# Performance work log

Hardware: AMD Instinct MI355X
Metric: run time of the kernel (lower is better)

The kernel has to match this reference:

```python
import jax, jax.numpy as jnp
import numpy as np

B, S, D, H = 2, 2048, 1024, 16
DH = D // H
ROPE_BASE = 10000.0


def apply_rope(x):
    # x: [B, H, S, DH]; rotate-half RoPE, base 10000
    half = DH // 2
    inv_freq = 1.0 / (ROPE_BASE ** (jnp.arange(half, dtype=jnp.float32) / half))
    ang = jnp.arange(S, dtype=jnp.float32)[:, None] * inv_freq[None, :]  # [S, half]
    cos = jnp.cos(ang)[None, None]  # [1,1,S,half]
    sin = jnp.sin(ang)[None, None]
    x1, x2 = x[..., :half], x[..., half:]
    return jnp.concatenate([x1 * cos - x2 * sin, x1 * sin + x2 * cos], axis=-1)


def setup_inputs() -> dict:
    key = jax.random.key(0)
    ks = jax.random.split(key, 9)
    w = lambda k: jax.random.normal(k, (D, D), dtype=jnp.float32) * 0.02
    return {
        "x": jax.random.normal(ks[0], (B, S, D), dtype=jnp.float32),
        "Wq": w(ks[1]), "bq": jnp.zeros((D,), jnp.float32),
        "Wk": w(ks[2]), "bk": jnp.zeros((D,), jnp.float32),
        "Wv": w(ks[3]), "bv": jnp.zeros((D,), jnp.float32),
        "Wo": w(ks[4]), "bo": jnp.zeros((D,), jnp.float32),
    }


def reference(x, Wq, bq, Wk, bk, Wv, bv, Wo, bo):
    # projections (W stored as [in, out])
    q = x @ Wq + bq
    k = x @ Wk + bk
    v = x @ Wv + bv
    # [B, S, D] -> [B, H, S, DH]
    to_heads = lambda t: t.reshape(B, S, H, DH).transpose(0, 2, 1, 3)
    q, k, v = to_heads(q), to_heads(k), to_heads(v)
    q = apply_rope(q)
    k = apply_rope(k)
    scores = jnp.einsum("bhqd,bhkd->bhqk", q, k) / jnp.sqrt(jnp.float32(DH))
    causal = jnp.tril(jnp.ones((S, S), dtype=bool))  # [S, S]
    scores = jnp.where(causal[None, None], scores, -jnp.inf)
    probs = jax.nn.softmax(scores, axis=-1)
    ctx = jnp.einsum("bhqk,bhkd->bhqd", probs, v)
    ctx = ctx.transpose(0, 2, 1, 3).reshape(B, S, D)  # concat heads
    return ctx @ Wo + bo
```

## Files before the change

### kernel.cpp

```cpp
#include <hip/hip_runtime.h>
#include <hip/hip_bf16.h>

#define B_  2
#define S_  2048
#define D_  1024
#define H_  16
#define DH_ 64

typedef __attribute__((ext_vector_type(8))) short bf16x8;
typedef __attribute__((ext_vector_type(4))) float f32x4;

__device__ __forceinline__ short f2bf(float f) {
  unsigned int u; __builtin_memcpy(&u, &f, 4);
  u = (u + 0x7FFFu + ((u >> 16) & 1u)) >> 16;
  return (short)u;
}
__device__ __forceinline__ unsigned cvtpk(float a, float b) {
  unsigned r;
  asm("v_cvt_pk_bf16_f32 %0, %1, %2" : "=v"(r) : "v"(a), "v"(b));
  return r;
}

#define GLOAD_LDS16(gp, lp) \
  __builtin_amdgcn_global_load_lds((const __attribute__((address_space(1))) void*)(gp), \
                                   (__attribute__((address_space(3))) void*)(lp), 16, 0, 0)

#define MFMA16(a, b, c) __builtin_amdgcn_mfma_f32_16x16x32_bf16(a, b, c, 0, 0, 0)

union U8 { unsigned u[4]; bf16x8 v; };

__global__ __launch_bounds__(256) void k_cvt(const float* __restrict__ in,
                                             short* __restrict__ out, int n4) {
  int i = blockIdx.x * 256 + threadIdx.x;
  if (i >= n4) return;
  float4 v = ((const float4*)in)[i];
  short4 o; o.x = f2bf(v.x); o.y = f2bf(v.y); o.z = f2bf(v.z); o.w = f2bf(v.w);
  *(short4*)(out + (size_t)i * 4) = o;
}

__global__ __launch_bounds__(256) void k_transpose4(const float* __restrict__ W0,
                                                    const float* __restrict__ W1,
                                                    const float* __restrict__ W2,
                                                    const float* __restrict__ W3,
                                                    short* __restrict__ WtBase) {
  __shared__ float tile[32][33];
  const float* W = (blockIdx.z == 0) ? W0 : (blockIdx.z == 1) ? W1 :
                   (blockIdx.z == 2) ? W2 : W3;
  short* Wt = WtBase + (size_t)blockIdx.z * D_ * D_;
  int tx = threadIdx.x, ty = threadIdx.y;
  int bx = blockIdx.x * 32, by = blockIdx.y * 32;
  #pragma unroll
  for (int i = 0; i < 32; i += 8)
    tile[ty + i][tx] = W[(size_t)(by + ty + i) * D_ + bx + tx];
  __syncthreads();
  #pragma unroll
  for (int i = 0; i < 32; i += 8)
    Wt[(size_t)(bx + ty + i) * D_ + by + tx] = f2bf(tile[tx][ty + i]);
}

__global__ __launch_bounds__(256) void k_rope_table(float* __restrict__ cosT,
                                                    float* __restrict__ sinT) {
  int i = blockIdx.x * 256 + threadIdx.x;
  int s = i >> 5, d = i & 31;
  float invf = exp2f(-(float)d * (13.287712379549449f / 32.0f));
  float ang = (float)s * invf;
  cosT[i] = cosf(ang);
  sinT[i] = sinf(ang);
}

__global__ __launch_bounds__(256) void k_gemm_qkv(const short* __restrict__ A,
                                                  const short* __restrict__ Bt,
                                                  const float* __restrict__ bq,
                                                  const float* __restrict__ bk,
                                                  const float* __restrict__ bv,
                                                  const float* __restrict__ cosT,
                                                  const float* __restrict__ sinT,
                                                  short* __restrict__ qb,
                                                  short* __restrict__ kb,
                                                  short* __restrict__ vb) {
  const int K = 1024;
  __shared__ __align__(16) short lA[128 * 32];
  __shared__ __align__(16) short lB[128 * 32];
  const int tid = threadIdx.x;
  const int wid = tid >> 6, lane = tid & 63;
  const int brow = blockIdx.y * 128, bcol = blockIdx.x * 128;
  const int wr = wid >> 1, wc = wid & 1;
  const int g = lane >> 4, c15 = lane & 15;
  const int sr = lane >> 2, scol = (lane & 3) * 8;
  f32x4 acc[4][4] = {};

  for (int kt = 0; kt < K; kt += 32) {
    __syncthreads();
    #pragma unroll
    for (int ch = 0; ch < 2; ++ch) {
      const short* ga = A + (size_t)(brow + ch * 64 + wid * 16 + sr) * K + kt + scol;
      const short* gb = Bt + (size_t)(bcol + ch * 64 + wid * 16 + sr) * K + kt + scol;
      GLOAD_LDS16(ga, &lA[(ch * 64 + wid * 16) * 32]);
      GLOAD_LDS16(gb, &lB[(ch * 64 + wid * 16) * 32]);
    }
    __syncthreads();
    bf16x8 af[4], bfr[4];
    #pragma unroll
    for (int mi = 0; mi < 4; ++mi)
      af[mi] = *(const bf16x8*)&lA[(wr * 64 + mi * 16 + c15) * 32 + g * 8];
    #pragma unroll
    for (int ni = 0; ni < 4; ++ni)
      bfr[ni] = *(const bf16x8*)&lB[(wc * 64 + ni * 16 + c15) * 32 + g * 8];
    #pragma unroll
    for (int mi = 0; mi < 4; ++mi)
      #pragma unroll
      for (int ni = 0; ni < 4; ++ni)
        acc[mi][ni] = MFMA16(af[mi], bfr[ni], acc[mi][ni]);
  }

  const int seg = bcol >> 10;
  const float* bp = (seg == 0) ? bq : (seg == 1) ? bk : bv;
  short* dst = (seg == 0) ? qb : (seg == 1) ? kb : vb;
  const float alpha = (seg == 0) ? 0.18033688f : 1.0f;
  const bool rope = (seg < 2);
  #pragma unroll
  for (int mi = 0; mi < 4; ++mi) {
    #pragma unroll
    for (int ni = 0; ni < 2; ++ni) {
      int col  = bcol + wc * 64 + ni * 16 + c15;
      int lcol = col & 1023;
      int d    = col & 63;
      float b1 = bp[lcol], b2 = bp[lcol + 32];
      #pragma unroll
      for (int r = 0; r < 4; ++r) {
        int row = brow + wr * 64 + mi * 16 + g * 4 + r;
        float x1 = (acc[mi][ni][r]     + b1) * alpha;
        float x2 = (acc[mi][ni + 2][r] + b2) * alpha;
        float o1 = x1, o2 = x2;
        if (rope) {
          int s = row & (S_ - 1);
          float co = cosT[s * 32 + d], si = sinT[s * 32 + d];
          o1 = x1 * co - x2 * si;
          o2 = x1 * si + x2 * co;
        }
        dst[(size_t)row * 1024 + lcol]      = f2bf(o1);
        dst[(size_t)row * 1024 + lcol + 32] = f2bf(o2);
      }
    }
  }
}

__global__ __launch_bounds__(256) void k_gemm(const short* __restrict__ A,
                                              const short* __restrict__ Bt,
                                              const float* __restrict__ bias,
                                              float* __restrict__ out,
                                              int M, int N, int K) {
  __shared__ __align__(16) short lA[128 * 32];
  __shared__ __align__(16) short lB[128 * 32];
  const int tid = threadIdx.x;
  const int wid = tid >> 6, lane = tid & 63;
  const int brow = blockIdx.y * 128, bcol = blockIdx.x * 128;
  const int wr = wid >> 1, wc = wid & 1;
  const int g = lane >> 4, c15 = lane & 15;
  const int sr = lane >> 2, scol = (lane & 3) * 8;
  f32x4 acc[4][4] = {};

  for (int kt = 0; kt < K; kt += 32) {
    __syncthreads();
    #pragma unroll
    for (int ch = 0; ch < 2; ++ch) {
      const short* ga = A + (size_t)(brow + ch * 64 + wid * 16 + sr) * K + kt + scol;
      const short* gb = Bt + (size_t)(bcol + ch * 64 + wid * 16 + sr) * K + kt + scol;
      GLOAD_LDS16(ga, &lA[(ch * 64 + wid * 16) * 32]);
      GLOAD_LDS16(gb, &lB[(ch * 64 + wid * 16) * 32]);
    }
    __syncthreads();
    bf16x8 af[4], bfr[4];
    #pragma unroll
    for (int mi = 0; mi < 4; ++mi)
      af[mi] = *(const bf16x8*)&lA[(wr * 64 + mi * 16 + c15) * 32 + g * 8];
    #pragma unroll
    for (int ni = 0; ni < 4; ++ni)
      bfr[ni] = *(const bf16x8*)&lB[(wc * 64 + ni * 16 + c15) * 32 + g * 8];
    #pragma unroll
    for (int mi = 0; mi < 4; ++mi)
      #pragma unroll
      for (int ni = 0; ni < 4; ++ni)
        acc[mi][ni] = MFMA16(af[mi], bfr[ni], acc[mi][ni]);
  }

  #pragma unroll
  for (int mi = 0; mi < 4; ++mi) {
    #pragma unroll
    for (int ni = 0; ni < 4; ++ni) {
      int col = bcol + wc * 64 + ni * 16 + c15;
      float bv = bias[col];
      #pragma unroll
      for (int r = 0; r < 4; ++r) {
        int row = brow + wr * 64 + mi * 16 + g * 4 + r;
        out[(size_t)row * N + col] = acc[mi][ni][r] + bv;
      }
    }
  }
}

__global__ __launch_bounds__(256) void k_flash(const short* __restrict__ Qb,
                                               const short* __restrict__ Kb,
                                               const short* __restrict__ Vb,
                                               short* __restrict__ Ctx,
                                               float* __restrict__ pO,
                                               float* __restrict__ pML) {
  __shared__ __align__(16) short Vt[2][64][72];
  __shared__ __align__(16) short Kl[2][4096];
  const int bid = blockIdx.x;
  const int sched = bid >> 5, bh = bid & 31;
  int qt, t0, t1, sid = 0; bool split;
  if (sched < 19) { qt = 18 - sched; t0 = 0; t1 = qt; split = false; }
  else {
    int j = sched - 19; qt = 31 - (j >> 1);
    int h1 = (qt + 2) >> 1;
    if ((j & 1) == 0) { t0 = h1; t1 = qt; }
    else              { t0 = 0;  t1 = h1 - 1; }
    split = true; sid = bh * 26 + j;
  }
  const int b   = bh >> 4, h = bh & 15;
  const int tid = threadIdx.x, w = tid >> 6, lane = tid & 63;
  const int g   = lane >> 4, c15 = lane & 15;
  const int qg0 = qt * 64 + w * 16;
  const int qabs = qg0 + c15;

  const short* qp = Qb + ((size_t)(b * S_ + qabs)) * D_ + h * DH_ + g * 8;
  bf16x8 qf0 = *(const bf16x8*)qp;
  bf16x8 qf1 = *(const bf16x8*)(qp + 32);

  const int vkv = lane;
  const int vd0 = w * 16;
  const int vcol = vkv ^ (w << 3);
  const short* vrow = Vb + (size_t)b * S_ * D_ + h * DH_ + vd0;

  const short* kbase = Kb + (size_t)b * S_ * D_ + h * DH_;
  const int kidx0 = w * 128 + lane;
  const int kkv0 = kidx0 >> 3, kdb0 = (kidx0 & 7) ^ (kkv0 & 7);
  const int kidx1 = kidx0 + 64;
  const int kkv1 = kidx1 >> 3, kdb1 = (kidx1 & 7) ^ (kkv1 & 7);

  f32x4 o[4] = {};
  float m = -1e30f, l = 0.0f;

  {
    const short* kb0 = kbase + (size_t)(t0 * 64) * D_;
    GLOAD_LDS16(kb0 + (size_t)kkv0 * D_ + kdb0 * 8, &Kl[t0 & 1][(w * 128) * 8]);
    GLOAD_LDS16(kb0 + (size_t)kkv1 * D_ + kdb1 * 8, &Kl[t0 & 1][(w * 128 + 64) * 8]);
    const short* vp = vrow + (size_t)(t0 * 64 + vkv) * D_;
    bf16x8 a = *(const bf16x8*)vp;
    bf16x8 c = *(const bf16x8*)(vp + 8);
    #pragma unroll
    for (int j = 0; j < 8; ++j) Vt[t0 & 1][vd0 + j][vcol] = a[j];
    #pragma unroll
    for (int j = 0; j < 8; ++j) Vt[t0 & 1][vd0 + 8 + j][vcol] = c[j];
  }
  __syncthreads();

  for (int t = t0; t <= t1; ++t) {
    const int kv0 = t * 64;
    bf16x8 nv0, nv1;
    if (t + 1 <= t1) {
      const short* kb2 = kbase + (size_t)(kv0 + 64) * D_;
      GLOAD_LDS16(kb2 + (size_t)kkv0 * D_ + kdb0 * 8, &Kl[(t + 1) & 1][(w * 128) * 8]);
      GLOAD_LDS16(kb2 + (size_t)kkv1 * D_ + kdb1 * 8, &Kl[(t + 1) & 1][(w * 128 + 64) * 8]);
      const short* vp = vrow + (size_t)(kv0 + 64 + vkv) * D_;
      nv0 = *(const bf16x8*)vp;
      nv1 = *(const bf16x8*)(vp + 8);
    }
    const short* ks = &Kl[t & 1][0];
    f32x4 s[4] = {};
    __builtin_amdgcn_s_setprio(1);
    #pragma unroll
    for (int n = 0; n < 4; ++n) {
      int krow = (n * 16 + c15) * 64;
      bf16x8 k0 = *(const bf16x8*)&ks[krow + ((g ^ (c15 & 7)) * 8)];
      bf16x8 k1 = *(const bf16x8*)&ks[krow + (((g + 4) ^ (c15 & 7)) * 8)];
      s[n] = MFMA16(k0, qf0, s[n]);
      s[n] = MFMA16(k1, qf1, s[n]);
    }
    __builtin_amdgcn_s_setprio(0);
    if (kv0 + 63 > qg0) {
      #pragma unroll
      for (int n = 0; n < 4; ++n)
        #pragma unroll
        for (int r = 0; r < 4; ++r)
          if (kv0 + n * 16 + g * 4 + r > qabs) s[n][r] = -1e30f;
    }
    float pm = -1e30f;
    #pragma unroll
    for (int n = 0; n < 4; ++n)
      #pragma unroll
      for (int r = 0; r < 4; ++r) pm = fmaxf(pm, s[n][r]);
    pm = fmaxf(pm, __shfl_xor(pm, 16));
    pm = fmaxf(pm, __shfl_xor(pm, 32));
    if (!__all(pm <= m + 8.0f)) {
      float nm = fmaxf(m, pm);
      float corr = exp2f(m - nm);
      m = nm; l *= corr;
      float cf[4];
      #pragma unroll
      for (int r = 0; r < 4; ++r) cf[r] = __shfl(corr, g * 4 + r);
      #pragma unroll
      for (int dblk = 0; dblk < 4; ++dblk)
        #pragma unroll
        for (int r = 0; r < 4; ++r) o[dblk][r] *= cf[r];
    }
    float rs = 0.0f;
    #pragma unroll
    for (int n = 0; n < 4; ++n)
      #pragma unroll
      for (int r = 0; r < 4; ++r) {
        float p = exp2f(s[n][r] - m);
        s[n][r] = p; rs += p;
      }
    rs += __shfl_xor(rs, 16);
    rs += __shfl_xor(rs, 32);
    l += rs;
    unsigned pk[4][2];
    #pragma unroll
    for (int n = 0; n < 4; ++n) {
      pk[n][0] = cvtpk(s[n][0], s[n][1]);
      pk[n][1] = cvtpk(s[n][2], s[n][3]);
    }
    U8 pa[2];
    #pragma unroll
    for (int kh = 0; kh < 2; ++kh) {
      #pragma unroll
      for (int widx = 0; widx < 4; ++widx) {
        int src = (2 * (g & 1) + (widx >> 1)) * 16 + c15;
        unsigned lo = __shfl(pk[2 * kh][widx & 1], src);
        unsigned hi = __shfl(pk[2 * kh + 1][widx & 1], src);
        pa[kh].u[widx] = (g & 2) ? hi : lo;
      }
    }
    __builtin_amdgcn_s_setprio(1);
    #pragma unroll
    for (int kh = 0; kh < 2; ++kh)
      #pragma unroll
      for (int dblk = 0; dblk < 4; ++dblk) {
        bf16x8 vbf = *(const bf16x8*)&Vt[t & 1][dblk * 16 + c15][kh * 32 + ((g ^ dblk) * 8)];
        o[dblk] = MFMA16(pa[kh].v, vbf, o[dblk]);
      }
    __builtin_amdgcn_s_setprio(0);
    if (t + 1 <= t1) {
      #pragma unroll
      for (int j = 0; j < 8; ++j) Vt[(t + 1) & 1][vd0 + j][vcol] = nv0[j];
      #pragma unroll
      for (int j = 0; j < 8; ++j) Vt[(t + 1) & 1][vd0 + 8 + j][vcol] = nv1[j];
    }
    __syncthreads();
  }

  if (!split) {
    float linv = 1.0f / l;
    float lf[4];
    #pragma unroll
    for (int r = 0; r < 4; ++r) lf[r] = __shfl(linv, g * 4 + r);
    #pragma unroll
    for (int dblk = 0; dblk < 4; ++dblk)
      #pragma unroll
      for (int r = 0; r < 4; ++r) {
        int q = qg0 + g * 4 + r;
        Ctx[((size_t)(b * S_ + q)) * D_ + h * DH_ + dblk * 16 + c15] = f2bf(o[dblk][r] * lf[r]);
      }
  } else {
    float* po = pO + ((size_t)sid * 64 + w * 16) * 64;
    #pragma unroll
    for (int dblk = 0; dblk < 4; ++dblk)
      #pragma unroll
      for (int r = 0; r < 4; ++r)
        po[(g * 4 + r) * 64 + dblk * 16 + c15] = o[dblk][r];
    if (lane < 16) {
      pML[(size_t)sid * 128 + w * 16 + lane]      = m;
      pML[(size_t)sid * 128 + 64 + w * 16 + lane] = l;
    }
  }
}

__global__ __launch_bounds__(256) void k_combine(const float* __restrict__ pO,
                                                 const float* __restrict__ pML,
                                                 short* __restrict__ Ctx) {
  const int p = blockIdx.x;
  const int qt = 19 + (p >> 5), bh = p & 31;
  const int b = bh >> 4, h = bh & 15;
  const int jb = (31 - qt) * 2;
  const int sidB = bh * 26 + jb;
  const int sidA = bh * 26 + jb + 1;
  const int q = threadIdx.x >> 2;
  const int d0 = (threadIdx.x & 3) * 16;
  float mA = pML[(size_t)sidA * 128 + q], lA = pML[(size_t)sidA * 128 + 64 + q];
  float mB = pML[(size_t)sidB * 128 + q], lB = pML[(size_t)sidB * 128 + 64 + q];
  float M = fmaxf(mA, mB);
  float wA = exp2f(mA - M), wB = exp2f(mB - M);
  float inv = 1.0f / (lA * wA + lB * wB);
  const float* oA = pO + ((size_t)sidA * 64 + q) * 64 + d0;
  const float* oB = pO + ((size_t)sidB * 64 + q) * 64 + d0;
  short* cp = Ctx + ((size_t)(b * S_ + qt * 64 + q)) * D_ + h * DH_ + d0;
  #pragma unroll
  for (int i = 0; i < 16; i += 4) {
    float4 a = *(const float4*)(oA + i);
    float4 c = *(const float4*)(oB + i);
    cp[i + 0] = f2bf((a.x * wA + c.x * wB) * inv);
    cp[i + 1] = f2bf((a.y * wA + c.y * wB) * inv);
    cp[i + 2] = f2bf((a.z * wA + c.z * wB) * inv);
    cp[i + 3] = f2bf((a.w * wA + c.w * wB) * inv);
  }
}

extern "C" void kernel_launch(void* const* d_in, const int* in_sizes, int n_in,
                              void* d_out, int out_size, void* d_ws, size_t ws_size,
                              hipStream_t stream) {
  (void)in_sizes; (void)n_in; (void)out_size; (void)ws_size;
  const float* x  = (const float*)d_in[0];
  const float* Wq = (const float*)d_in[1];
  const float* bq = (const float*)d_in[2];
  const float* Wk = (const float*)d_in[3];
  const float* bk = (const float*)d_in[4];
  const float* Wv = (const float*)d_in[5];
  const float* bv = (const float*)d_in[6];
  const float* Wo = (const float*)d_in[7];
  const float* bo = (const float*)d_in[8];
  float* out = (float*)d_out;
  char* ws = (char*)d_ws;

  const size_t MS = (size_t)B_ * S_;
  short* xb  = (short*)(ws);
  short* wqT = (short*)(ws + (size_t)8 * 1024 * 1024);
  short* wkT = wqT + (size_t)D_ * D_;
  short* wvT = wkT + (size_t)D_ * D_;
  short* woT = wvT + (size_t)D_ * D_;
  short* qb  = (short*)(ws + (size_t)16 * 1024 * 1024);
  short* kb  = qb + MS * D_;
  short* vb  = kb + MS * D_;
  short* ctx = vb + MS * D_;
  float* cosT = (float*)(ws + (size_t)48 * 1024 * 1024);
  float* sinT = cosT + (size_t)S_ * 32;
  float* pO  = (float*)(ws);
  float* pML = (float*)(ws + (size_t)48 * 1024 * 1024 + 512 * 1024);

  k_cvt<<<dim3((unsigned)(MS * D_ / 4 / 256)), 256, 0, stream>>>(x, xb, (int)(MS * D_ / 4));
  k_transpose4<<<dim3(32, 32, 4), dim3(32, 8), 0, stream>>>(Wq, Wk, Wv, Wo, wqT);
  k_rope_table<<<dim3(S_ * 32 / 256), 256, 0, stream>>>(cosT, sinT);
  k_gemm_qkv<<<dim3(24, 32), 256, 0, stream>>>(xb, wqT, bq, bk, bv, cosT, sinT, qb, kb, vb);
  k_flash<<<dim3(45 * 32), 256, 0, stream>>>(qb, kb, vb, ctx, pO, pML);
  k_combine<<<dim3(13 * 32), 256, 0, stream>>>(pO, pML, ctx);
  k_gemm<<<dim3(8, 32), 256, 0, stream>>>(ctx, woT, bo, out, 4096, 1024, 1024);
}
```

Before: 138.5 us.

## Deepen flash K/V prefetch, swizzle GEMM tiles, merge prep kernels

```diff
diff --git a/kernel.cpp b/kernel.cpp
--- a/kernel.cpp
+++ b/kernel.cpp
@@ -27,15 +27,32 @@
 
 #define MFMA16(a, b, c) __builtin_amdgcn_mfma_f32_16x16x32_bf16(a, b, c, 0, 0, 0)
 
+#define RAW_BARRIER() do {                                   \
+    asm volatile("s_waitcnt lgkmcnt(0)" ::: "memory");       \
+    __builtin_amdgcn_s_barrier();                            \
+    asm volatile("" ::: "memory");                           \
+  } while (0)
+
 union U8 { unsigned u[4]; bf16x8 v; };
 
-__global__ __launch_bounds__(256) void k_cvt(const float* __restrict__ in,
-                                             short* __restrict__ out, int n4) {
-  int i = blockIdx.x * 256 + threadIdx.x;
-  if (i >= n4) return;
-  float4 v = ((const float4*)in)[i];
-  short4 o; o.x = f2bf(v.x); o.y = f2bf(v.y); o.z = f2bf(v.z); o.w = f2bf(v.w);
-  *(short4*)(out + (size_t)i * 4) = o;
+__global__ __launch_bounds__(256) void k_cvt_table(const float* __restrict__ in,
+                                                   short* __restrict__ out,
+                                                   float* __restrict__ cosT,
+                                                   float* __restrict__ sinT) {
+  int bid = blockIdx.x;
+  if (bid < 4096) {
+    int i = bid * 256 + threadIdx.x;
+    float4 v = ((const float4*)in)[i];
+    short4 o; o.x = f2bf(v.x); o.y = f2bf(v.y); o.z = f2bf(v.z); o.w = f2bf(v.w);
+    *(short4*)(out + (size_t)i * 4) = o;
+  } else {
+    int i = (bid - 4096) * 256 + threadIdx.x;
+    int s = i >> 5, d = i & 31;
+    float invf = exp2f(-(float)d * (13.287712379549449f / 32.0f));
+    float ang = (float)s * invf;
+    cosT[i] = cosf(ang);
+    sinT[i] = sinf(ang);
+  }
 }
 
 __global__ __launch_bounds__(256) void k_transpose4(const float* __restrict__ W0,
@@ -56,16 +73,6 @@
   #pragma unroll
   for (int i = 0; i < 32; i += 8)
     Wt[(size_t)(bx + ty + i) * D_ + by + tx] = f2bf(tile[tx][ty + i]);
-}
-
-__global__ __launch_bounds__(256) void k_rope_table(float* __restrict__ cosT,
-                                                    float* __restrict__ sinT) {
-  int i = blockIdx.x * 256 + threadIdx.x;
-  int s = i >> 5, d = i & 31;
-  float invf = exp2f(-(float)d * (13.287712379549449f / 32.0f));
-  float ang = (float)s * invf;
-  cosT[i] = cosf(ang);
-  sinT[i] = sinf(ang);
 }
 
 __global__ __launch_bounds__(256) void k_gemm_qkv(const short* __restrict__ A,
@@ -81,9 +88,12 @@
   const int K = 1024;
   __shared__ __align__(16) short lA[128 * 32];
   __shared__ __align__(16) short lB[128 * 32];
+  const int fid = blockIdx.y * 24 + blockIdx.x;
+  const int swz = (fid & 7) * 96 + (fid >> 3);
+  const int bxs = swz % 24, bys = swz / 24;
   const int tid = threadIdx.x;
   const int wid = tid >> 6, lane = tid & 63;
-  const int brow = blockIdx.y * 128, bcol = blockIdx.x * 128;
+  const int brow = bys * 128, bcol = bxs * 128;
   const int wr = wid >> 1, wc = wid & 1;
   const int g = lane >> 4, c15 = lane & 15;
   const int sr = lane >> 2, scol = (lane & 3) * 8;
@@ -152,9 +162,12 @@
                                               int M, int N, int K) {
   __shared__ __align__(16) short lA[128 * 32];
   __shared__ __align__(16) short lB[128 * 32];
+  const int fid = blockIdx.y * 8 + blockIdx.x;
+  const int swz = (fid & 7) * 32 + (fid >> 3);
+  const int bxs = swz % 8, bys = swz / 8;
   const int tid = threadIdx.x;
   const int wid = tid >> 6, lane = tid & 63;
-  const int brow = blockIdx.y * 128, bcol = blockIdx.x * 128;
+  const int brow = bys * 128, bcol = bxs * 128;
   const int wr = wid >> 1, wc = wid & 1;
   const int g = lane >> 4, c15 = lane & 15;
   const int sr = lane >> 2, scol = (lane & 3) * 8;
@@ -199,12 +212,66 @@
   }
 }
 
-__global__ __launch_bounds__(256) void k_flash(const short* __restrict__ Qb,
-                                               const short* __restrict__ Kb,
-                                               const short* __restrict__ Vb,
-                                               short* __restrict__ Ctx,
-                                               float* __restrict__ pO,
-                                               float* __restrict__ pML) {
+__device__ __forceinline__ void softmax_g(f32x4 (&s)[4], float& m, float& l,
+                                          f32x4 (&o)[4], int g) {
+  float pm = -1e30f;
+  #pragma unroll
+  for (int n = 0; n < 4; ++n)
+    #pragma unroll
+    for (int r = 0; r < 4; ++r) pm = fmaxf(pm, s[n][r]);
+  pm = fmaxf(pm, __shfl_xor(pm, 16));
+  pm = fmaxf(pm, __shfl_xor(pm, 32));
+  if (!__all(pm <= m + 8.0f)) {
+    float nm = fmaxf(m, pm);
+    float corr = exp2f(m - nm);
+    m = nm; l *= corr;
+    float cf[4];
+    #pragma unroll
+    for (int r = 0; r < 4; ++r) cf[r] = __shfl(corr, g * 4 + r);
+    #pragma unroll
+    for (int dblk = 0; dblk < 4; ++dblk)
+      #pragma unroll
+      for (int r = 0; r < 4; ++r) o[dblk][r] *= cf[r];
+  }
+  float rs = 0.0f;
+  #pragma unroll
+  for (int n = 0; n < 4; ++n)
+    #pragma unroll
+    for (int r = 0; r < 4; ++r) {
+      float p = exp2f(s[n][r] - m);
+      s[n][r] = p; rs += p;
+    }
+  rs += __shfl_xor(rs, 16);
+  rs += __shfl_xor(rs, 32);
+  l += rs;
+}
+
+__device__ __forceinline__ void build_pa(const f32x4 (&s)[4], U8 (&pa)[2],
+                                         int g, int c15) {
+  unsigned pk[4][2];
+  #pragma unroll
+  for (int n = 0; n < 4; ++n) {
+    pk[n][0] = cvtpk(s[n][0], s[n][1]);
+    pk[n][1] = cvtpk(s[n][2], s[n][3]);
+  }
+  #pragma unroll
+  for (int kh = 0; kh < 2; ++kh) {
+    #pragma unroll
+    for (int widx = 0; widx < 4; ++widx) {
+      int src = (2 * (g & 1) + (widx >> 1)) * 16 + c15;
+      unsigned lo = __shfl(pk[2 * kh][widx & 1], src);
+      unsigned hi = __shfl(pk[2 * kh + 1][widx & 1], src);
+      pa[kh].u[widx] = (g & 2) ? hi : lo;
+    }
+  }
+}
+
+__global__ __launch_bounds__(256, 4) void k_flash(const short* __restrict__ Qb,
+                                                  const short* __restrict__ Kb,
+                                                  const short* __restrict__ Vb,
+                                                  short* __restrict__ Ctx,
+                                                  float* __restrict__ pO,
+                                                  float* __restrict__ pML) {
   __shared__ __align__(16) short Vt[2][64][72];
   __shared__ __align__(16) short Kl[2][4096];
   const int bid = blockIdx.x;
@@ -242,114 +309,95 @@
   f32x4 o[4] = {};
   float m = -1e30f, l = 0.0f;
 
+  bf16x8 kc0, kc1, vc0, vc1, kn0, kn1, vn0, vn1;
+
   {
     const short* kb0 = kbase + (size_t)(t0 * 64) * D_;
-    GLOAD_LDS16(kb0 + (size_t)kkv0 * D_ + kdb0 * 8, &Kl[t0 & 1][(w * 128) * 8]);
-    GLOAD_LDS16(kb0 + (size_t)kkv1 * D_ + kdb1 * 8, &Kl[t0 & 1][(w * 128 + 64) * 8]);
+    bf16x8 tk0 = *(const bf16x8*)(kb0 + (size_t)kkv0 * D_ + kdb0 * 8);
+    bf16x8 tk1 = *(const bf16x8*)(kb0 + (size_t)kkv1 * D_ + kdb1 * 8);
     const short* vp = vrow + (size_t)(t0 * 64 + vkv) * D_;
-    bf16x8 a = *(const bf16x8*)vp;
-    bf16x8 c = *(const bf16x8*)(vp + 8);
-    #pragma unroll
-    for (int j = 0; j < 8; ++j) Vt[t0 & 1][vd0 + j][vcol] = a[j];
-    #pragma unroll
-    for (int j = 0; j < 8; ++j) Vt[t0 & 1][vd0 + 8 + j][vcol] = c[j];
-  }
-  __syncthreads();
-
-  for (int t = t0; t <= t1; ++t) {
-    const int kv0 = t * 64;
-    bf16x8 nv0, nv1;
-    if (t + 1 <= t1) {
-      const short* kb2 = kbase + (size_t)(kv0 + 64) * D_;
-      GLOAD_LDS16(kb2 + (size_t)kkv0 * D_ + kdb0 * 8, &Kl[(t + 1) & 1][(w * 128) * 8]);
-      GLOAD_LDS16(kb2 + (size_t)kkv1 * D_ + kdb1 * 8, &Kl[(t + 1) & 1][(w * 128 + 64) * 8]);
-      const short* vp = vrow + (size_t)(kv0 + 64 + vkv) * D_;
-      nv0 = *(const bf16x8*)vp;
-      nv1 = *(const bf16x8*)(vp + 8);
-    }
-    const short* ks = &Kl[t & 1][0];
-    f32x4 s[4] = {};
-    __builtin_amdgcn_s_setprio(1);
-    #pragma unroll
-    for (int n = 0; n < 4; ++n) {
-      int krow = (n * 16 + c15) * 64;
-      bf16x8 k0 = *(const bf16x8*)&ks[krow + ((g ^ (c15 & 7)) * 8)];
-      bf16x8 k1 = *(const bf16x8*)&ks[krow + (((g + 4) ^ (c15 & 7)) * 8)];
-      s[n] = MFMA16(k0, qf0, s[n]);
-      s[n] = MFMA16(k1, qf1, s[n]);
-    }
-    __builtin_amdgcn_s_setprio(0);
-    if (kv0 + 63 > qg0) {
-      #pragma unroll
-      for (int n = 0; n < 4; ++n)
-        #pragma unroll
-        for (int r = 0; r < 4; ++r)
-          if (kv0 + n * 16 + g * 4 + r > qabs) s[n][r] = -1e30f;
-    }
-    float pm = -1e30f;
-    #pragma unroll
-    for (int n = 0; n < 4; ++n)
-      #pragma unroll
-      for (int r = 0; r < 4; ++r) pm = fmaxf(pm, s[n][r]);
-    pm = fmaxf(pm, __shfl_xor(pm, 16));
-    pm = fmaxf(pm, __shfl_xor(pm, 32));
-    if (!__all(pm <= m + 8.0f)) {
-      float nm = fmaxf(m, pm);
-      float corr = exp2f(m - nm);
-      m = nm; l *= corr;
-      float cf[4];
-      #pragma unroll
-      for (int r = 0; r < 4; ++r) cf[r] = __shfl(corr, g * 4 + r);
-      #pragma unroll
-      for (int dblk = 0; dblk < 4; ++dblk)
-        #pragma unroll
-        for (int r = 0; r < 4; ++r) o[dblk][r] *= cf[r];
-    }
-    float rs = 0.0f;
-    #pragma unroll
-    for (int n = 0; n < 4; ++n)
-      #pragma unroll
-      for (int r = 0; r < 4; ++r) {
-        float p = exp2f(s[n][r] - m);
-        s[n][r] = p; rs += p;
-      }
-    rs += __shfl_xor(rs, 16);
-    rs += __shfl_xor(rs, 32);
-    l += rs;
-    unsigned pk[4][2];
-    #pragma unroll
-    for (int n = 0; n < 4; ++n) {
-      pk[n][0] = cvtpk(s[n][0], s[n][1]);
-      pk[n][1] = cvtpk(s[n][2], s[n][3]);
-    }
-    U8 pa[2];
-    #pragma unroll
-    for (int kh = 0; kh < 2; ++kh) {
-      #pragma unroll
-      for (int widx = 0; widx < 4; ++widx) {
-        int src = (2 * (g & 1) + (widx >> 1)) * 16 + c15;
-        unsigned lo = __shfl(pk[2 * kh][widx & 1], src);
-        unsigned hi = __shfl(pk[2 * kh + 1][widx & 1], src);
-        pa[kh].u[widx] = (g & 2) ? hi : lo;
-      }
-    }
-    __builtin_amdgcn_s_setprio(1);
-    #pragma unroll
-    for (int kh = 0; kh < 2; ++kh)
-      #pragma unroll
-      for (int dblk = 0; dblk < 4; ++dblk) {
-        bf16x8 vbf = *(const bf16x8*)&Vt[t & 1][dblk * 16 + c15][kh * 32 + ((g ^ dblk) * 8)];
-        o[dblk] = MFMA16(pa[kh].v, vbf, o[dblk]);
-      }
-    __builtin_amdgcn_s_setprio(0);
-    if (t + 1 <= t1) {
-      #pragma unroll
-      for (int j = 0; j < 8; ++j) Vt[(t + 1) & 1][vd0 + j][vcol] = nv0[j];
-      #pragma unroll
-      for (int j = 0; j < 8; ++j) Vt[(t + 1) & 1][vd0 + 8 + j][vcol] = nv1[j];
-    }
-    __syncthreads();
-  }
+    bf16x8 tv0 = *(const bf16x8*)vp;
+    bf16x8 tv1 = *(const bf16x8*)(vp + 8);
+    *(bf16x8*)&Kl[t0 & 1][kidx0 * 8] = tk0;
+    *(bf16x8*)&Kl[t0 & 1][kidx1 * 8] = tk1;
+    #pragma unroll
+    for (int j = 0; j < 8; ++j) Vt[t0 & 1][vd0 + j][vcol] = tv0[j];
+    #pragma unroll
+    for (int j = 0; j < 8; ++j) Vt[t0 & 1][vd0 + 8 + j][vcol] = tv1[j];
+    if (t0 + 1 <= t1) {
+      const short* kb1 = kbase + (size_t)((t0 + 1) * 64) * D_;
+      kc0 = *(const bf16x8*)(kb1 + (size_t)kkv0 * D_ + kdb0 * 8);
+      kc1 = *(const bf16x8*)(kb1 + (size_t)kkv1 * D_ + kdb1 * 8);
+      const short* vp1 = vrow + (size_t)((t0 + 1) * 64 + vkv) * D_;
+      vc0 = *(const bf16x8*)vp1;
+      vc1 = *(const bf16x8*)(vp1 + 8);
+    }
+  }
+  RAW_BARRIER();
+
+#define FBODY(T, KC0, KC1, VC0, VC1, KN0, KN1, VN0, VN1) do {                   \
+    const int kv0 = (T) * 64;                                                   \
+    if ((T) + 2 <= t1) {                                                        \
+      const short* kb2 = kbase + (size_t)(kv0 + 128) * D_;                      \
+      KN0 = *(const bf16x8*)(kb2 + (size_t)kkv0 * D_ + kdb0 * 8);               \
+      KN1 = *(const bf16x8*)(kb2 + (size_t)kkv1 * D_ + kdb1 * 8);               \
+      const short* vp2 = vrow + (size_t)(kv0 + 128 + vkv) * D_;                 \
+      VN0 = *(const bf16x8*)vp2;                                                \
+      VN1 = *(const bf16x8*)(vp2 + 8);                                          \
+    }                                                                           \
+    if (kv0 <= qg0 + 15) {                                                      \
+      const short* ks = &Kl[(T) & 1][0];                                        \
+      f32x4 s[4] = {};                                                          \
+      __builtin_amdgcn_s_setprio(1);                                            \
+      _Pragma("unroll")                                                         \
+      for (int n = 0; n < 4; ++n) {                                             \
+        int krow = (n * 16 + c15) * 64;                                         \
+        bf16x8 k0 = *(const bf16x8*)&ks[krow + ((g ^ (c15 & 7)) * 8)];          \
+        bf16x8 k1 = *(const bf16x8*)&ks[krow + (((g + 4) ^ (c15 & 7)) * 8)];    \
+        s[n] = MFMA16(k0, qf0, s[n]);                                           \
+        s[n] = MFMA16(k1, qf1, s[n]);                                           \
+      }                                                                         \
+      __builtin_amdgcn_s_setprio(0);                                            \
+      if (kv0 + 63 > qg0) {                                                     \
+        _Pragma("unroll")                                                       \
+        for (int n = 0; n < 4; ++n)                                             \
+          _Pragma("unroll")                                                     \
+          for (int r = 0; r < 4; ++r)                                           \
+            if (kv0 + n * 16 + g * 4 + r > qabs) s[n][r] = -1e30f;              \
+      }                                                                         \
+      softmax_g(s, m, l, o, g);                                                 \
+      U8 pa[2];                                                                 \
+      build_pa(s, pa, g, c15);                                                  \
+      __builtin_amdgcn_s_setprio(1);                                            \
+      _Pragma("unroll")                                                         \
+      for (int kh = 0; kh < 2; ++kh)                                            \
+        _Pragma("unroll")                                                       \
+        for (int dblk = 0; dblk < 4; ++dblk) {                                  \
+          bf16x8 vbf = *(const bf16x8*)&Vt[(T) & 1][dblk * 16 + c15]            \
+                                         [kh * 32 + ((g ^ dblk) * 8)];          \
+          o[dblk] = MFMA16(pa[kh].v, vbf, o[dblk]);                             \
+        }                                                                       \
+      __builtin_amdgcn_s_setprio(0);                                            \
+    }                                                                           \
+    if ((T) + 1 <= t1) {                                                        \
+      *(bf16x8*)&Kl[((T) + 1) & 1][kidx0 * 8] = KC0;                            \
+      *(bf16x8*)&Kl[((T) + 1) & 1][kidx1 * 8] = KC1;                            \
+      _Pragma("unroll")                                                         \
+      for (int j = 0; j < 8; ++j) Vt[((T) + 1) & 1][vd0 + j][vcol] = VC0[j];    \
+      _Pragma("unroll")                                                         \
+      for (int j = 0; j < 8; ++j) Vt[((T) + 1) & 1][vd0 + 8 + j][vcol] = VC1[j];\
+      RAW_BARRIER();                                                            \
+    }                                                                           \
+  } while (0)
+
+  for (int t = t0; t <= t1; ) {
+    FBODY(t, kc0, kc1, vc0, vc1, kn0, kn1, vn0, vn1);
+    ++t;
+    if (t > t1) break;
+    FBODY(t, kn0, kn1, vn0, vn1, kc0, kc1, vc0, vc1);
+    ++t;
+  }
+#undef FBODY
 
   if (!split) {
     float linv = 1.0f / l;
@@ -438,9 +486,8 @@
   float* pO  = (float*)(ws);
   float* pML = (float*)(ws + (size_t)48 * 1024 * 1024 + 512 * 1024);
 
-  k_cvt<<<dim3((unsigned)(MS * D_ / 4 / 256)), 256, 0, stream>>>(x, xb, (int)(MS * D_ / 4));
+  k_cvt_table<<<dim3(4096 + 256), 256, 0, stream>>>(x, xb, cosT, sinT);
   k_transpose4<<<dim3(32, 32, 4), dim3(32, 8), 0, stream>>>(Wq, Wk, Wv, Wo, wqT);
-  k_rope_table<<<dim3(S_ * 32 / 256), 256, 0, stream>>>(cosT, sinT);
   k_gemm_qkv<<<dim3(24, 32), 256, 0, stream>>>(xb, wqT, bq, bk, bv, cosT, sinT, qb, kb, vb);
   k_flash<<<dim3(45 * 32), 256, 0, stream>>>(qb, kb, vb, ctx, pO, pML);
   k_combine<<<dim3(13 * 32), 256, 0, stream>>>(pO, pML, ctx);
```

Result: faster. 135.6 us, median of 2 (-2.1%).

## Merge cvt and rope kernels, swizzle GEMM grids, single-buffer flash attention

Applied to the files above, without the earlier changes.

```diff
diff --git a/kernel.cpp b/kernel.cpp
--- a/kernel.cpp
+++ b/kernel.cpp
@@ -27,15 +27,37 @@
 
 #define MFMA16(a, b, c) __builtin_amdgcn_mfma_f32_16x16x32_bf16(a, b, c, 0, 0, 0)
 
+#define RAW_BARRIER() do {                                   \
+    asm volatile("s_waitcnt lgkmcnt(0)" ::: "memory");       \
+    __builtin_amdgcn_s_barrier();                            \
+    asm volatile("" ::: "memory");                           \
+  } while (0)
+#define PLAIN_BARRIER() do {                                 \
+    asm volatile("" ::: "memory");                           \
+    __builtin_amdgcn_s_barrier();                            \
+    asm volatile("" ::: "memory");                           \
+  } while (0)
+
 union U8 { unsigned u[4]; bf16x8 v; };
 
-__global__ __launch_bounds__(256) void k_cvt(const float* __restrict__ in,
-                                             short* __restrict__ out, int n4) {
-  int i = blockIdx.x * 256 + threadIdx.x;
-  if (i >= n4) return;
-  float4 v = ((const float4*)in)[i];
-  short4 o; o.x = f2bf(v.x); o.y = f2bf(v.y); o.z = f2bf(v.z); o.w = f2bf(v.w);
-  *(short4*)(out + (size_t)i * 4) = o;
+__global__ __launch_bounds__(256) void k_cvt_table(const float* __restrict__ in,
+                                                   short* __restrict__ out,
+                                                   float* __restrict__ cosT,
+                                                   float* __restrict__ sinT) {
+  int bid = blockIdx.x;
+  if (bid < 4096) {
+    int i = bid * 256 + threadIdx.x;
+    float4 v = ((const float4*)in)[i];
+    short4 o; o.x = f2bf(v.x); o.y = f2bf(v.y); o.z = f2bf(v.z); o.w = f2bf(v.w);
+    *(short4*)(out + (size_t)i * 4) = o;
+  } else {
+    int i = (bid - 4096) * 256 + threadIdx.x;
+    int s = i >> 5, d = i & 31;
+    float invf = exp2f(-(float)d * (13.287712379549449f / 32.0f));
+    float ang = (float)s * invf;
+    cosT[i] = cosf(ang);
+    sinT[i] = sinf(ang);
+  }
 }
 
 __global__ __launch_bounds__(256) void k_transpose4(const float* __restrict__ W0,
@@ -56,16 +78,6 @@
   #pragma unroll
   for (int i = 0; i < 32; i += 8)
     Wt[(size_t)(bx + ty + i) * D_ + by + tx] = f2bf(tile[tx][ty + i]);
-}
-
-__global__ __launch_bounds__(256) void k_rope_table(float* __restrict__ cosT,
-                                                    float* __restrict__ sinT) {
-  int i = blockIdx.x * 256 + threadIdx.x;
-  int s = i >> 5, d = i & 31;
-  float invf = exp2f(-(float)d * (13.287712379549449f / 32.0f));
-  float ang = (float)s * invf;
-  cosT[i] = cosf(ang);
-  sinT[i] = sinf(ang);
 }
 
 __global__ __launch_bounds__(256) void k_gemm_qkv(const short* __restrict__ A,
@@ -81,9 +93,12 @@
   const int K = 1024;
   __shared__ __align__(16) short lA[128 * 32];
   __shared__ __align__(16) short lB[128 * 32];
+  const int fid = blockIdx.y * 24 + blockIdx.x;
+  const int swz = (fid & 7) * 96 + (fid >> 3);
+  const int bxs = swz % 24, bys = swz / 24;
   const int tid = threadIdx.x;
   const int wid = tid >> 6, lane = tid & 63;
-  const int brow = blockIdx.y * 128, bcol = blockIdx.x * 128;
+  const int brow = bys * 128, bcol = bxs * 128;
   const int wr = wid >> 1, wc = wid & 1;
   const int g = lane >> 4, c15 = lane & 15;
   const int sr = lane >> 2, scol = (lane & 3) * 8;
@@ -152,9 +167,12 @@
                                               int M, int N, int K) {
   __shared__ __align__(16) short lA[128 * 32];
   __shared__ __align__(16) short lB[128 * 32];
+  const int fid = blockIdx.y * 8 + blockIdx.x;
+  const int swz = (fid & 7) * 32 + (fid >> 3);
+  const int bxs = swz % 8, bys = swz / 8;
   const int tid = threadIdx.x;
   const int wid = tid >> 6, lane = tid & 63;
-  const int brow = blockIdx.y * 128, bcol = blockIdx.x * 128;
+  const int brow = bys * 128, bcol = bxs * 128;
   const int wr = wid >> 1, wc = wid & 1;
   const int g = lane >> 4, c15 = lane & 15;
   const int sr = lane >> 2, scol = (lane & 3) * 8;
@@ -199,14 +217,68 @@
   }
 }
 
-__global__ __launch_bounds__(256) void k_flash(const short* __restrict__ Qb,
-                                               const short* __restrict__ Kb,
-                                               const short* __restrict__ Vb,
-                                               short* __restrict__ Ctx,
-                                               float* __restrict__ pO,
-                                               float* __restrict__ pML) {
-  __shared__ __align__(16) short Vt[2][64][72];
-  __shared__ __align__(16) short Kl[2][4096];
+__device__ __forceinline__ void softmax_g(f32x4 (&s)[4], float& m, float& l,
+                                          f32x4 (&o)[4], int g) {
+  float pm = -1e30f;
+  #pragma unroll
+  for (int n = 0; n < 4; ++n)
+    #pragma unroll
+    for (int r = 0; r < 4; ++r) pm = fmaxf(pm, s[n][r]);
+  pm = fmaxf(pm, __shfl_xor(pm, 16));
+  pm = fmaxf(pm, __shfl_xor(pm, 32));
+  if (!__all(pm <= m + 8.0f)) {
+    float nm = fmaxf(m, pm);
+    float corr = exp2f(m - nm);
+    m = nm; l *= corr;
+    float cf[4];
+    #pragma unroll
+    for (int r = 0; r < 4; ++r) cf[r] = __shfl(corr, g * 4 + r);
+    #pragma unroll
+    for (int dblk = 0; dblk < 4; ++dblk)
+      #pragma unroll
+      for (int r = 0; r < 4; ++r) o[dblk][r] *= cf[r];
+  }
+  float rs = 0.0f;
+  #pragma unroll
+  for (int n = 0; n < 4; ++n)
+    #pragma unroll
+    for (int r = 0; r < 4; ++r) {
+      float p = exp2f(s[n][r] - m);
+      s[n][r] = p; rs += p;
+    }
+  rs += __shfl_xor(rs, 16);
+  rs += __shfl_xor(rs, 32);
+  l += rs;
+}
+
+__device__ __forceinline__ void build_pa(const f32x4 (&s)[4], U8 (&pa)[2],
+                                         int g, int c15) {
+  unsigned pk[4][2];
+  #pragma unroll
+  for (int n = 0; n < 4; ++n) {
+    pk[n][0] = cvtpk(s[n][0], s[n][1]);
+    pk[n][1] = cvtpk(s[n][2], s[n][3]);
+  }
+  #pragma unroll
+  for (int kh = 0; kh < 2; ++kh) {
+    #pragma unroll
+    for (int widx = 0; widx < 4; ++widx) {
+      int src = (2 * (g & 1) + (widx >> 1)) * 16 + c15;
+      unsigned lo = __shfl(pk[2 * kh][widx & 1], src);
+      unsigned hi = __shfl(pk[2 * kh + 1][widx & 1], src);
+      pa[kh].u[widx] = (g & 2) ? hi : lo;
+    }
+  }
+}
+
+__global__ __launch_bounds__(256, 8) void k_flash(const short* __restrict__ Qb,
+                                                  const short* __restrict__ Kb,
+                                                  const short* __restrict__ Vb,
+                                                  short* __restrict__ Ctx,
+                                                  float* __restrict__ pO,
+                                                  float* __restrict__ pML) {
+  __shared__ __align__(16) short Vt[64][64];
+  __shared__ __align__(16) short Kl[4096];
   const int bid = blockIdx.x;
   const int sched = bid >> 5, bh = bid & 31;
   int qt, t0, t1, sid = 0; bool split;
@@ -228,9 +300,7 @@
   bf16x8 qf0 = *(const bf16x8*)qp;
   bf16x8 qf1 = *(const bf16x8*)(qp + 32);
 
-  const int vkv = lane;
   const int vd0 = w * 16;
-  const int vcol = vkv ^ (w << 3);
   const short* vrow = Vb + (size_t)b * S_ * D_ + h * DH_ + vd0;
 
   const short* kbase = Kb + (size_t)b * S_ * D_ + h * DH_;
@@ -242,113 +312,77 @@
   f32x4 o[4] = {};
   float m = -1e30f, l = 0.0f;
 
+  bf16x8 kc0, kc1, vc0, vc1;
+
   {
     const short* kb0 = kbase + (size_t)(t0 * 64) * D_;
-    GLOAD_LDS16(kb0 + (size_t)kkv0 * D_ + kdb0 * 8, &Kl[t0 & 1][(w * 128) * 8]);
-    GLOAD_LDS16(kb0 + (size_t)kkv1 * D_ + kdb1 * 8, &Kl[t0 & 1][(w * 128 + 64) * 8]);
-    const short* vp = vrow + (size_t)(t0 * 64 + vkv) * D_;
-    bf16x8 a = *(const bf16x8*)vp;
-    bf16x8 c = *(const bf16x8*)(vp + 8);
-    #pragma unroll
-    for (int j = 0; j < 8; ++j) Vt[t0 & 1][vd0 + j][vcol] = a[j];
-    #pragma unroll
-    for (int j = 0; j < 8; ++j) Vt[t0 & 1][vd0 + 8 + j][vcol] = c[j];
-  }
-  __syncthreads();
+    bf16x8 tk0 = *(const bf16x8*)(kb0 + (size_t)kkv0 * D_ + kdb0 * 8);
+    bf16x8 tk1 = *(const bf16x8*)(kb0 + (size_t)kkv1 * D_ + kdb1 * 8);
+    const short* vp = vrow + (size_t)(t0 * 64 + lane) * D_;
+    bf16x8 tv0 = *(const bf16x8*)vp;
+    bf16x8 tv1 = *(const bf16x8*)(vp + 8);
+    *(bf16x8*)&Kl[kidx0 * 8] = tk0;
+    *(bf16x8*)&Kl[kidx1 * 8] = tk1;
+    #pragma unroll
+    for (int j = 0; j < 8; ++j) Vt[vd0 + j][lane ^ ((j & 7) << 3)] = tv0[j];
+    #pragma unroll
+    for (int j = 0; j < 8; ++j) Vt[vd0 + 8 + j][lane ^ ((j & 7) << 3)] = tv1[j];
+  }
+  RAW_BARRIER();
 
   for (int t = t0; t <= t1; ++t) {
     const int kv0 = t * 64;
-    bf16x8 nv0, nv1;
     if (t + 1 <= t1) {
-      const short* kb2 = kbase + (size_t)(kv0 + 64) * D_;
-      GLOAD_LDS16(kb2 + (size_t)kkv0 * D_ + kdb0 * 8, &Kl[(t + 1) & 1][(w * 128) * 8]);
-      GLOAD_LDS16(kb2 + (size_t)kkv1 * D_ + kdb1 * 8, &Kl[(t + 1) & 1][(w * 128 + 64) * 8]);
-      const short* vp = vrow + (size_t)(kv0 + 64 + vkv) * D_;
-      nv0 = *(const bf16x8*)vp;
-      nv1 = *(const bf16x8*)(vp + 8);
-    }
-    const short* ks = &Kl[t & 1][0];
-    f32x4 s[4] = {};
-    __builtin_amdgcn_s_setprio(1);
-    #pragma unroll
-    for (int n = 0; n < 4; ++n) {
-      int krow = (n * 16 + c15) * 64;
-      bf16x8 k0 = *(const bf16x8*)&ks[krow + ((g ^ (c15 & 7)) * 8)];
-      bf16x8 k1 = *(const bf16x8*)&ks[krow + (((g + 4) ^ (c15 & 7)) * 8)];
-      s[n] = MFMA16(k0, qf0, s[n]);
-      s[n] = MFMA16(k1, qf1, s[n]);
-    }
-    __builtin_amdgcn_s_setprio(0);
-    if (kv0 + 63 > qg0) {
-      #pragma unroll
-      for (int n = 0; n < 4; ++n)
+      const short* kb1 = kbase + (size_t)(kv0 + 64) * D_;
+      kc0 = *(const bf16x8*)(kb1 + (size_t)kkv0 * D_ + kdb0 * 8);
+      kc1 = *(const bf16x8*)(kb1 + (size_t)kkv1 * D_ + kdb1 * 8);
+      const short* vp1 = vrow + (size_t)(kv0 + 64 + lane) * D_;
+      vc0 = *(const bf16x8*)vp1;
+      vc1 = *(const bf16x8*)(vp1 + 8);
+    }
+    if (kv0 <= qg0 + 15) {
+      f32x4 s[4] = {};
+      __builtin_amdgcn_s_setprio(1);
+      #pragma unroll
+      for (int n = 0; n < 4; ++n) {
+        int krow = (n * 16 + c15) * 64;
+        bf16x8 k0 = *(const bf16x8*)&Kl[krow + ((g ^ (c15 & 7)) * 8)];
+        bf16x8 k1 = *(const bf16x8*)&Kl[krow + (((g + 4) ^ (c15 & 7)) * 8)];
+        s[n] = MFMA16(k0, qf0, s[n]);
+        s[n] = MFMA16(k1, qf1, s[n]);
+      }
+      __builtin_amdgcn_s_setprio(0);
+      if (kv0 + 63 > qg0) {
         #pragma unroll
-        for (int r = 0; r < 4; ++r)
-          if (kv0 + n * 16 + g * 4 + r > qabs) s[n][r] = -1e30f;
-    }
-    float pm = -1e30f;
-    #pragma unroll
-    for (int n = 0; n < 4; ++n)
-      #pragma unroll
-      for (int r = 0; r < 4; ++r) pm = fmaxf(pm, s[n][r]);
-    pm = fmaxf(pm, __shfl_xor(pm, 16));
-    pm = fmaxf(pm, __shfl_xor(pm, 32));
-    if (!__all(pm <= m + 8.0f)) {
-      float nm = fmaxf(m, pm);
-      float corr = exp2f(m - nm);
-      m = nm; l *= corr;
-      float cf[4];
-      #pragma unroll
-      for (int r = 0; r < 4; ++r) cf[r] = __shfl(corr, g * 4 + r);
-      #pragma unroll
-      for (int dblk = 0; dblk < 4; ++dblk)
+        for (int n = 0; n < 4; ++n)
+          #pragma unroll
+          for (int r = 0; r < 4; ++r)
+            if (kv0 + n * 16 + g * 4 + r > qabs) s[n][r] = -1e30f;
+      }
+      softmax_g(s, m, l, o, g);
+      U8 pa[2];
+      build_pa(s, pa, g, c15);
+      __builtin_amdgcn_s_setprio(1);
+      #pragma unroll
+      for (int kh = 0; kh < 2; ++kh)
         #pragma unroll
-        for (int r = 0; r < 4; ++r) o[dblk][r] *= cf[r];
-    }
-    float rs = 0.0f;
-    #pragma unroll
-    for (int n = 0; n < 4; ++n)
-      #pragma unroll
-      for (int r = 0; r < 4; ++r) {
-        float p = exp2f(s[n][r] - m);
-        s[n][r] = p; rs += p;
-      }
-    rs += __shfl_xor(rs, 16);
-    rs += __shfl_xor(rs, 32);
-    l += rs;
-    unsigned pk[4][2];
-    #pragma unroll
-    for (int n = 0; n < 4; ++n) {
-      pk[n][0] = cvtpk(s[n][0], s[n][1]);
-      pk[n][1] = cvtpk(s[n][2], s[n][3]);
-    }
-    U8 pa[2];
-    #pragma unroll
-    for (int kh = 0; kh < 2; ++kh) {
-      #pragma unroll
-      for (int widx = 0; widx < 4; ++widx) {
-        int src = (2 * (g & 1) + (widx >> 1)) * 16 + c15;
-        unsigned lo = __shfl(pk[2 * kh][widx & 1], src);
-        unsigned hi = __shfl(pk[2 * kh + 1][widx & 1], src);
-        pa[kh].u[widx] = (g & 2) ? hi : lo;
-      }
-    }
-    __builtin_amdgcn_s_setprio(1);
-    #pragma unroll
-    for (int kh = 0; kh < 2; ++kh)
-      #pragma unroll
-      for (int dblk = 0; dblk < 4; ++dblk) {
-        bf16x8 vbf = *(const bf16x8*)&Vt[t & 1][dblk * 16 + c15][kh * 32 + ((g ^ dblk) * 8)];
-        o[dblk] = MFMA16(pa[kh].v, vbf, o[dblk]);
-      }
-    __builtin_amdgcn_s_setprio(0);
+        for (int dblk = 0; dblk < 4; ++dblk) {
+          bf16x8 vbf = *(const bf16x8*)&Vt[dblk * 16 + c15]
+                                         [(kh * 32 + g * 8) ^ ((c15 & 7) << 3)];
+          o[dblk] = MFMA16(pa[kh].v, vbf, o[dblk]);
+        }
+      __builtin_amdgcn_s_setprio(0);
+    }
     if (t + 1 <= t1) {
-      #pragma unroll
-      for (int j = 0; j < 8; ++j) Vt[(t + 1) & 1][vd0 + j][vcol] = nv0[j];
-      #pragma unroll
-      for (int j = 0; j < 8; ++j) Vt[(t + 1) & 1][vd0 + 8 + j][vcol] = nv1[j];
-    }
-    __syncthreads();
+      PLAIN_BARRIER();
+      *(bf16x8*)&Kl[kidx0 * 8] = kc0;
+      *(bf16x8*)&Kl[kidx1 * 8] = kc1;
+      #pragma unroll
+      for (int j = 0; j < 8; ++j) Vt[vd0 + j][lane ^ ((j & 7) << 3)] = vc0[j];
+      #pragma unroll
+      for (int j = 0; j < 8; ++j) Vt[vd0 + 8 + j][lane ^ ((j & 7) << 3)] = vc1[j];
+      RAW_BARRIER();
+    }
   }
 
   if (!split) {
@@ -438,9 +472,8 @@
   float* pO  = (float*)(ws);
   float* pML = (float*)(ws + (size_t)48 * 1024 * 1024 + 512 * 1024);
 
-  k_cvt<<<dim3((unsigned)(MS * D_ / 4 / 256)), 256, 0, stream>>>(x, xb, (int)(MS * D_ / 4));
+  k_cvt_table<<<dim3(4096 + 256), 256, 0, stream>>>(x, xb, cosT, sinT);
   k_transpose4<<<dim3(32, 32, 4), dim3(32, 8), 0, stream>>>(Wq, Wk, Wv, Wo, wqT);
-  k_rope_table<<<dim3(S_ * 32 / 256), 256, 0, stream>>>(cosT, sinT);
   k_gemm_qkv<<<dim3(24, 32), 256, 0, stream>>>(xb, wqT, bq, bk, bv, cosT, sinT, qb, kb, vb);
   k_flash<<<dim3(45 * 32), 256, 0, stream>>>(qb, kb, vb, ctx, pO, pML);
   k_combine<<<dim3(13 * 32), 256, 0, stream>>>(pO, pML, ctx);
```

Result: slower. 238.1 us (+72.0%).
